# Kernel optimization log

Measured on AMD Instinct MI355X. Metric: run time of the kernel, lower is better.

## Reference

```python
import jax, jax.numpy as jnp
import numpy as np

NUM_HEADS = 8
WINDOW = 3
LOCAL_LEN = WINDOW * WINDOW
SR_RATIO = 8


def _normalize(v, eps=1e-12):
    n = jnp.linalg.norm(v, axis=-1, keepdims=True)
    return v / jnp.maximum(n, eps)


def _layernorm(v, g, b, eps=1e-5):
    m = v.mean(-1, keepdims=True)
    var = ((v - m) ** 2).mean(-1, keepdims=True)
    return (v - m) / jnp.sqrt(var + eps) * g + b


def _unfold3(x, H, W):
    # x: [B, C, H, W] -> [B, C, 9, H*W]  (kernel 3, pad 1, stride 1; torch nn.Unfold layout)
    B, C = x.shape[0], x.shape[1]
    xp = jnp.pad(x, ((0, 0), (0, 0), (1, 1), (1, 1)))
    patches = jnp.stack([xp[:, :, di:di + H, dj:dj + W]
                         for di in range(WINDOW) for dj in range(WINDOW)], axis=2)
    return patches.reshape(B, C, LOCAL_LEN, H * W)


def _forward(x, relative_coords_table, seq_length_scale, q_w, q_b, kv_w, kv_b,
             temperature, query_embedding, sr_w, sr_b, norm_g, norm_b,
             cpb_fc1_w, cpb_fc1_b, cpb_fc2_w, cpb_fc2_b,
             rel_bias_local, learnable_tokens, learnable_bias,
             proj_w, proj_b, relative_pos_index, padding_mask, H, W):
    B, N, C = x.shape
    hd = C // NUM_HEADS
    pool_H, pool_W = H // SR_RATIO, W // SR_RATIO
    pool_len = pool_H * pool_W

    # ---- queries ----
    q = (x @ q_w.T + q_b).reshape(B, N, NUM_HEADS, hd).transpose(0, 2, 1, 3)  # [B,h,N,d]
    q_norm = _normalize(q)
    q_scaled = (q_norm + query_embedding) * jax.nn.softplus(temperature) * seq_length_scale

    # ---- local k/v via unfold ----
    kv = x @ kv_w.T + kv_b  # [B,N,2C]
    k_loc = _normalize(kv[..., :C].reshape(B, N, NUM_HEADS, hd)).reshape(B, N, C)
    kv_img = jnp.concatenate([k_loc, kv[..., C:]], -1).transpose(0, 2, 1).reshape(B, 2 * C, H, W)
    kv_unf = _unfold3(kv_img, H, W).reshape(B, 2 * NUM_HEADS, hd, LOCAL_LEN, N)
    kv_unf = kv_unf.transpose(0, 1, 4, 2, 3)  # [B,2h,N,d,9]
    k_local, v_local = kv_unf[:, :NUM_HEADS], kv_unf[:, NUM_HEADS:]

    attn_local = jnp.einsum('bhnd,bhndl->bhnl', q_scaled, k_local) + rel_bias_local[:, None, :]
    attn_local = jnp.where(padding_mask, -jnp.inf, attn_local)

    # ---- pooled global k/v ----
    x_img = x.transpose(0, 2, 1).reshape(B, C, H, W)
    x_sr = jax.nn.gelu(jnp.einsum('oc,bchw->bohw', sr_w, x_img) + sr_b[None, :, None, None],
                       approximate=False)
    x_pool = x_sr.reshape(B, C, pool_H, SR_RATIO, pool_W, SR_RATIO).mean((3, 5))
    x_pool = x_pool.reshape(B, C, pool_len).transpose(0, 2, 1)
    x_pool = _layernorm(x_pool, norm_g, norm_b)
    kv_p = (x_pool @ kv_w.T + kv_b).reshape(B, pool_len, 2 * NUM_HEADS, hd).transpose(0, 2, 1, 3)
    k_pool, v_pool = kv_p[:, :NUM_HEADS], kv_p[:, NUM_HEADS:]

    # ---- continuous relative position bias (extrapolation path) ----
    cpb = jax.nn.relu(relative_coords_table @ cpb_fc1_w.T + cpb_fc1_b) @ cpb_fc2_w.T + cpb_fc2_b  # [T,h]
    pool_bias = cpb[relative_pos_index].reshape(N, pool_len, NUM_HEADS).transpose(2, 0, 1)  # [h,N,P]

    attn_pool = jnp.einsum('bhnd,bhpd->bhnp', q_scaled, _normalize(k_pool)) + pool_bias

    attn = jax.nn.softmax(jnp.concatenate([attn_local, attn_pool], -1), axis=-1)
    a_loc, a_pool = attn[..., :LOCAL_LEN], attn[..., LOCAL_LEN:]

    lt = jnp.einsum('bhnd,hdl->bhnl', q_norm, learnable_tokens) + learnable_bias + a_loc
    x_local = jnp.einsum('bhnl,bhndl->bhnd', lt, v_local)
    x_p = jnp.einsum('bhnp,bhpd->bhnd', a_pool, v_pool)
    out = (x_local + x_p).transpose(0, 2, 1, 3).reshape(B, N, C)
    return out @ proj_w.T + proj_b


def setup_inputs() -> dict:
    key = jax.random.key(0)
    B, H, W, C = 4, 64, 64, 256
    N = H * W
    hd = C // NUM_HEADS
    pool_H, pool_W = H // SR_RATIO, W // SR_RATIO
    pool_len = pool_H * pool_W

    # padding mask + per-query valid window length (get_seqlen_and_mask)
    ii, jj = np.meshgrid(np.arange(H), np.arange(W), indexing='ij')
    cols = []
    for di in range(WINDOW):
        for dj in range(WINDOW):
            ni, nj = ii + di - 1, jj + dj - 1
            cols.append(((ni < 0) | (ni >= H) | (nj < 0) | (nj >= W)).reshape(-1))
    padding_mask = np.stack(cols, -1)  # [N, 9], True = outside image
    local_len = (~padding_mask).sum(-1, keepdims=True).astype(np.float32)
    seq_length_scale = np.log(local_len + pool_len)  # [N, 1]

    # get_relative_position_cpb((H,W), (pool_H,pool_W))
    axis_q = np.arange(H, dtype=np.float64)
    axis_k = axis_q.reshape(pool_H, SR_RATIO).mean(-1)
    kh, kw = np.meshgrid(axis_k, axis_k, indexing='ij')
    qh, qw = np.meshgrid(axis_q, axis_q, indexing='ij')
    rel_h = (qh.ravel()[:, None] - kh.ravel()[None, :]) / (H - 1) * 8
    rel_w = (qw.ravel()[:, None] - kw.ravel()[None, :]) / (W - 1) * 8
    rel = np.stack([rel_h, rel_w], -1).reshape(-1, 2)
    table, idx = np.unique(rel, axis=0, return_inverse=True)
    table = np.sign(table) * np.log2(np.abs(table) + 1.0) / np.log2(8.0)

    ks = jax.random.split(key, 12)

    def nrm(k, shape, std=0.02):
        return jax.random.normal(k, shape, jnp.float32) * std

    return {
        'x': jax.random.normal(ks[0], (B, N, C), jnp.float32),
        'relative_coords_table': jnp.asarray(table, jnp.float32),
        'seq_length_scale': jnp.asarray(seq_length_scale, jnp.float32),
        'q_w': nrm(ks[1], (C, C)), 'q_b': jnp.zeros((C,), jnp.float32),
        'kv_w': nrm(ks[2], (2 * C, C)), 'kv_b': jnp.zeros((2 * C,), jnp.float32),
        'temperature': jnp.full((NUM_HEADS, 1, 1), float(np.log(np.expm1(1.0 / 0.24))), jnp.float32),
        'query_embedding': nrm(ks[3], (NUM_HEADS, 1, hd)),
        'sr_w': nrm(ks[4], (C, C)), 'sr_b': jnp.zeros((C,), jnp.float32),
        'norm_g': jnp.ones((C,), jnp.float32), 'norm_b': jnp.zeros((C,), jnp.float32),
        'cpb_fc1_w': nrm(ks[5], (512, 2), 0.1), 'cpb_fc1_b': jnp.zeros((512,), jnp.float32),
        'cpb_fc2_w': nrm(ks[6], (NUM_HEADS, 512)), 'cpb_fc2_b': jnp.zeros((NUM_HEADS,), jnp.float32),
        'rel_bias_local': nrm(ks[7], (NUM_HEADS, LOCAL_LEN), 0.0004),
        'learnable_tokens': nrm(ks[8], (NUM_HEADS, hd, LOCAL_LEN)),
        'learnable_bias': jnp.zeros((NUM_HEADS, 1, LOCAL_LEN), jnp.float32),
        'proj_w': nrm(ks[9], (C, C)), 'proj_b': jnp.zeros((C,), jnp.float32),
        'relative_pos_index': jnp.asarray(idx, jnp.int32),
        'padding_mask': jnp.asarray(padding_mask),
        'H': H, 'W': W,
    }


def reference(x, relative_coords_table, seq_length_scale, q_w, q_b, kv_w, kv_b,
              temperature, query_embedding, sr_w, sr_b, norm_g, norm_b,
              cpb_fc1_w, cpb_fc1_b, cpb_fc2_w, cpb_fc2_b,
              rel_bias_local, learnable_tokens, learnable_bias,
              proj_w, proj_b, relative_pos_index, padding_mask, H, W):
    return _forward(x, relative_coords_table, seq_length_scale, q_w, q_b, kv_w, kv_b,
                    temperature, query_embedding, sr_w, sr_b, norm_g, norm_b,
                    cpb_fc1_w, cpb_fc1_b, cpb_fc2_w, cpb_fc2_b,
                    rel_bias_local, learnable_tokens, learnable_bias,
                    proj_w, proj_b, relative_pos_index, padding_mask, H, W)
```

## Files before the change

### kernel.cpp

```cpp
#include <hip/hip_runtime.h>
#include <math.h>


typedef unsigned short ushort_t;
typedef __attribute__((ext_vector_type(8))) _Float16 half8;
typedef __attribute__((ext_vector_type(2))) _Float16 half2_t;
typedef __attribute__((ext_vector_type(4))) float f32x4;

static __device__ __forceinline__ ushort_t f2h(float f) {
    _Float16 h = (_Float16)f;
    return *(ushort_t*)&h;
}

static __device__ __forceinline__ float fdot2f(half2_t a, half2_t b, float c) {
#if __has_builtin(__builtin_amdgcn_fdot2)
    return __builtin_amdgcn_fdot2(a, b, c, false);
#else
    return (float)a[0] * (float)b[0] + (float)a[1] * (float)b[1] + c;
#endif
}

#define GLOAD16(g, l)                                                        \
    __builtin_amdgcn_global_load_lds(                                        \
        (const __attribute__((address_space(1))) unsigned int*)(g),          \
        (__attribute__((address_space(3))) unsigned int*)(l), 16, 0, 0)

template <int TM>
__global__ __launch_bounds__(256) void mfma_hgemm(
    const ushort_t* __restrict__ Ag, const ushort_t* __restrict__ Bg,
    const float* __restrict__ bias, float* __restrict__ out0,
    ushort_t* __restrict__ qh_out, ushort_t* __restrict__ kvh,
    ushort_t* __restrict__ xsrh, int mode)
{
    const int K = 256;
    const int IM = TM / 32;
    __shared__ ushort_t Ah[TM * 32];
    __shared__ ushort_t Bh[64 * 32];

    const int t = threadIdx.x;
    const int w = t >> 6;
    const int lane = t & 63;
    const int bm = blockIdx.y * TM;
    const int bn = blockIdx.x * 64;
    const int wm = (w >> 1) * (TM / 2);
    const int wn = (w & 1) * 32;

    f32x4 acc[IM][2];
#pragma unroll
    for (int i = 0; i < IM; ++i)
#pragma unroll
        for (int j = 0; j < 2; ++j) acc[i][j] = f32x4{0.f, 0.f, 0.f, 0.f};

    const int lrow = t >> 2;
    const int lk8  = (t & 3) * 8;

    for (int k0 = 0; k0 < K; k0 += 32) {
#pragma unroll
        for (int r = 0; r < TM / 64; ++r) {
            GLOAD16(Ag + (size_t)(bm + r * 64 + lrow) * K + k0 + lk8,
                    &Ah[(unsigned)(r * 64 + (w * 16)) * 32]);
        }
        GLOAD16(Bg + (size_t)(bn + lrow) * K + k0 + lk8,
                &Bh[(unsigned)(w * 16) * 32]);
        __syncthreads();

        const int fr = lane & 15;
        const int fq = (lane >> 4) * 8;
        half8 af[IM], bf[2];
#pragma unroll
        for (int i = 0; i < IM; ++i)
            af[i] = *(const half8*)&Ah[(wm + i * 16 + fr) * 32 + fq];
#pragma unroll
        for (int j = 0; j < 2; ++j)
            bf[j] = *(const half8*)&Bh[(wn + j * 16 + fr) * 32 + fq];
#pragma unroll
        for (int i = 0; i < IM; ++i)
#pragma unroll
            for (int j = 0; j < 2; ++j)
                acc[i][j] = __builtin_amdgcn_mfma_f32_16x16x32_f16(af[i], bf[j], acc[i][j], 0, 0, 0);
        __syncthreads();
    }

    const int fr = lane & 15;
    const int q4 = (lane >> 4) * 4;
#pragma unroll
    for (int i = 0; i < IM; ++i) {
#pragma unroll
        for (int r = 0; r < 4; ++r) {
            const int row = bm + wm + i * 16 + q4 + r;
            const int col0 = bn + wn + fr;
            const int col1 = col0 + 16;
            float v0 = acc[i][0][r] + bias[col0];
            float v1 = acc[i][1][r] + bias[col1];
            if (mode == 0) {
                if (col0 < 256) {
                    qh_out[(size_t)row * 256 + col0] = f2h(v0);
                    qh_out[(size_t)row * 256 + col1] = f2h(v1);
                } else if (col0 < 512) {
                    float ss = v0 * v0 + v1 * v1;
                    ss += __shfl_xor(ss, 1); ss += __shfl_xor(ss, 2);
                    ss += __shfl_xor(ss, 4); ss += __shfl_xor(ss, 8);
                    const float invn = 1.0f / fmaxf(sqrtf(ss), 1e-12f);
                    kvh[(size_t)row * 512 + (col0 - 256)] = f2h(v0 * invn);
                    kvh[(size_t)row * 512 + (col1 - 256)] = f2h(v1 * invn);
                } else if (col0 < 768) {
                    kvh[(size_t)row * 512 + (col0 - 256)] = f2h(v0);
                    kvh[(size_t)row * 512 + (col1 - 256)] = f2h(v1);
                } else {
                    v0 = 0.5f * v0 * (1.0f + erff(v0 * 0.70710678118654752f));
                    v1 = 0.5f * v1 * (1.0f + erff(v1 * 0.70710678118654752f));
                    xsrh[(size_t)row * 256 + (col0 - 768)] = f2h(v0);
                    xsrh[(size_t)row * 256 + (col1 - 768)] = f2h(v1);
                }
            } else {
                out0[(size_t)row * 256 + col0] = v0;
                out0[(size_t)row * 256 + col1] = v1;
            }
        }
    }
}

__global__ __launch_bounds__(256) void prep(
    const float4* __restrict__ x, ushort4* __restrict__ xh, int n4,
    const float* __restrict__ qw, const float* __restrict__ kvw,
    const float* __restrict__ srw, const float* __restrict__ pw,
    const float* __restrict__ qb, const float* __restrict__ kvb,
    const float* __restrict__ srb,
    ushort_t* __restrict__ Wall, ushort_t* __restrict__ Pw,
    float* __restrict__ ball)
{
    int idx = blockIdx.x * 256 + threadIdx.x;
    if (idx < n4) {
        float4 v = x[idx];
        ushort4 h;
        h.x = f2h(v.x); h.y = f2h(v.y); h.z = f2h(v.z); h.w = f2h(v.w);
        xh[idx] = h;
    }
    if (idx < 262144) {
        int nn = idx >> 8, k = idx & 255;
        float a;
        if (nn < 256)      a = qw[nn * 256 + k];
        else if (nn < 768) a = kvw[(nn - 256) * 256 + k];
        else               a = srw[(nn - 768) * 256 + k];
        Wall[idx] = f2h(a);
    }
    if (idx < 65536) Pw[idx] = f2h(pw[idx]);
    if (idx < 1024) {
        float bv;
        if (idx < 256)      bv = qb[idx];
        else if (idx < 768) bv = kvb[idx - 256];
        else                bv = srb[idx - 768];
        ball[idx] = bv;
    }
}

__global__ __launch_bounds__(256) void bias_expand_t(
    const int* __restrict__ rpi, const float* __restrict__ cpbT,
    float* __restrict__ pbias)
{
    int idx = blockIdx.x * 256 + threadIdx.x;
    int h = idx >> 18;
    int np = idx & 262143;
    pbias[idx] = cpbT[(size_t)rpi[np] * 8 + h];
}

#define BM 64
#define BN 64
#define BKK 16
__global__ __launch_bounds__(256) void gemm_bias_act(
    const float* __restrict__ A, const float* __restrict__ Wt,
    const float* __restrict__ bias, float* __restrict__ Cmat,
    int M, int N, int K, int act)
{
    __shared__ float As[BKK][BM + 4];
    __shared__ float Bs[BKK][BN + 4];
    const int tid = threadIdx.x;
    const int bm = blockIdx.y * BM;
    const int bn = blockIdx.x * BN;
    const int tr = (tid >> 4) << 2;
    const int tc = (tid & 15) << 2;
    const int lr = tid >> 2;
    const int lc = (tid & 3) << 2;
    float acc[4][4] = {{0.f}};

    for (int k0 = 0; k0 < K; k0 += BKK) {
        float4 av = *(const float4*)(A  + (size_t)(bm + lr) * K + k0 + lc);
        float4 wv = *(const float4*)(Wt + (size_t)(bn + lr) * K + k0 + lc);
        As[lc + 0][lr] = av.x; As[lc + 1][lr] = av.y;
        As[lc + 2][lr] = av.z; As[lc + 3][lr] = av.w;
        Bs[lc + 0][lr] = wv.x; Bs[lc + 1][lr] = wv.y;
        Bs[lc + 2][lr] = wv.z; Bs[lc + 3][lr] = wv.w;
        __syncthreads();
#pragma unroll
        for (int kk = 0; kk < BKK; ++kk) {
            float4 a  = *(const float4*)&As[kk][tr];
            float4 bq = *(const float4*)&Bs[kk][tc];
            float av4[4] = {a.x, a.y, a.z, a.w};
            float bv4[4] = {bq.x, bq.y, bq.z, bq.w};
#pragma unroll
            for (int ii = 0; ii < 4; ++ii)
#pragma unroll
                for (int jj = 0; jj < 4; ++jj)
                    acc[ii][jj] = fmaf(av4[ii], bv4[jj], acc[ii][jj]);
        }
        __syncthreads();
    }
#pragma unroll
    for (int ii = 0; ii < 4; ++ii) {
        int m = bm + tr + ii;
#pragma unroll
        for (int jj = 0; jj < 4; ++jj) {
            int nn = bn + tc + jj;
            float v = acc[ii][jj] + bias[nn];
            if (act == 1) v = 0.5f * v * (1.0f + erff(v * 0.70710678118654752f));
            Cmat[(size_t)m * N + nn] = v;
        }
    }
}

__global__ __launch_bounds__(256) void headnorm(float* __restrict__ buf, int rowStride)
{
    size_t row = blockIdx.x;
    int tid = threadIdx.x;
    float* p = buf + row * (size_t)rowStride + tid;
    float v = *p;
    float ss = v * v;
#pragma unroll
    for (int off = 16; off; off >>= 1) ss += __shfl_xor(ss, off, 32);
    *p = v / fmaxf(sqrtf(ss), 1e-12f);
}

__global__ __launch_bounds__(256) void pool_ln(
    const ushort_t* __restrict__ xsr, const float* __restrict__ g,
    const float* __restrict__ be, float* __restrict__ xpool, int Hh, int Ww)
{
    const int C = 256;
    const int Nn = Hh * Ww;
    int b = blockIdx.x >> 6;
    int pidx = blockIdx.x & 63;
    int ph = pidx >> 3, pw = pidx & 7;
    int tid = threadIdx.x;
    float s = 0.f;
    for (int si = 0; si < 8; ++si) {
        int i = ph * 8 + si;
        const ushort_t* rowp = xsr + ((size_t)b * Nn + (size_t)i * Ww + pw * 8) * C + tid;
#pragma unroll
        for (int sj = 0; sj < 8; ++sj)
            s += (float)(*(const _Float16*)&rowp[(size_t)sj * C]);
    }
    s *= (1.f / 64.f);
    __shared__ float red[256];
    red[tid] = s; __syncthreads();
    for (int st = 128; st; st >>= 1) { if (tid < st) red[tid] += red[tid + st]; __syncthreads(); }
    float mean = red[0] * (1.f / 256.f);
    __syncthreads();
    float dv = s - mean;
    red[tid] = dv * dv; __syncthreads();
    for (int st = 128; st; st >>= 1) { if (tid < st) red[tid] += red[tid + st]; __syncthreads(); }
    float var = red[0] * (1.f / 256.f);
    xpool[(size_t)blockIdx.x * C + tid] = dv * rsqrtf(var + 1e-5f) * g[tid] + be[tid];
}

__global__ __launch_bounds__(256) void cpb_mlp_v2(
    const float* __restrict__ table, const float* __restrict__ w1,
    const float* __restrict__ b1, const float* __restrict__ w2,
    const float* __restrict__ b2, float* __restrict__ outc, int T)
{
    const int wv = threadIdx.x >> 6;
    const int lane = threadIdx.x & 63;
    const int row = blockIdx.x * 4 + wv;
    if (row >= T) return;
    const float t0 = table[(size_t)row * 2];
    const float t1 = table[(size_t)row * 2 + 1];
    const int base = lane * 8;

    const float4* w1p = (const float4*)(w1 + (size_t)base * 2);
    float4 wa = w1p[0], wb = w1p[1], wc = w1p[2], wd = w1p[3];
    float4 ba = *(const float4*)(b1 + base);
    float4 bb = *(const float4*)(b1 + base + 4);
    float h[8];
    h[0] = fmaxf(fmaf(t1, wa.y, fmaf(t0, wa.x, ba.x)), 0.f);
    h[1] = fmaxf(fmaf(t1, wa.w, fmaf(t0, wa.z, ba.y)), 0.f);
    h[2] = fmaxf(fmaf(t1, wb.y, fmaf(t0, wb.x, ba.z)), 0.f);
    h[3] = fmaxf(fmaf(t1, wb.w, fmaf(t0, wb.z, ba.w)), 0.f);
    h[4] = fmaxf(fmaf(t1, wc.y, fmaf(t0, wc.x, bb.x)), 0.f);
    h[5] = fmaxf(fmaf(t1, wc.w, fmaf(t0, wc.z, bb.y)), 0.f);
    h[6] = fmaxf(fmaf(t1, wd.y, fmaf(t0, wd.x, bb.z)), 0.f);
    h[7] = fmaxf(fmaf(t1, wd.w, fmaf(t0, wd.z, bb.w)), 0.f);

#pragma unroll
    for (int hh = 0; hh < 8; ++hh) {
        const float4* w2p = (const float4*)(w2 + (size_t)hh * 512 + base);
        float4 p0 = w2p[0], p1 = w2p[1];
        float s = h[0]*p0.x + h[1]*p0.y + h[2]*p0.z + h[3]*p0.w
                + h[4]*p1.x + h[5]*p1.y + h[6]*p1.z + h[7]*p1.w;
#pragma unroll
        for (int off = 1; off <= 32; off <<= 1) s += __shfl_xor(s, off);
        if (lane == 0) outc[(size_t)row * 8 + hh] = s + b2[hh];
    }
}

__global__ __launch_bounds__(256) void attn_v7(
    const ushort_t* __restrict__ qh_g,
    const ushort_t* __restrict__ kvh,
    const float* __restrict__ kvp,
    const float* __restrict__ pbias,
    const float* __restrict__ sls, const float* __restrict__ temp,
    const float* __restrict__ qe, const float* __restrict__ rbl,
    const float* __restrict__ ltok, const float* __restrict__ lbias,
    ushort_t* __restrict__ attno_hf)
{
    const int h = blockIdx.y, b = blockIdx.z;
    const int t = threadIdx.x;

    __shared__ half8 kp_s[64][4];
    __shared__ half8 vp_s[64][4];
    __shared__ float lts[9][32];
    __shared__ float rbl_s[9], lb_s[9], qe_s[32];

    {
        const int p = t >> 2;
        const int g4 = t & 3;
        const float* g = kvp + ((size_t)(b * 64 + p)) * 512 + h * 32 + g4 * 8;
        float4 ka = *(const float4*)(g + 0);
        float4 kb = *(const float4*)(g + 4);
        float4 va = *(const float4*)(g + 256);
        float4 vb = *(const float4*)(g + 260);
        half8 kh, vh;
        kh[0]=(_Float16)ka.x; kh[1]=(_Float16)ka.y; kh[2]=(_Float16)ka.z; kh[3]=(_Float16)ka.w;
        kh[4]=(_Float16)kb.x; kh[5]=(_Float16)kb.y; kh[6]=(_Float16)kb.z; kh[7]=(_Float16)kb.w;
        vh[0]=(_Float16)va.x; vh[1]=(_Float16)va.y; vh[2]=(_Float16)va.z; vh[3]=(_Float16)va.w;
        vh[4]=(_Float16)vb.x; vh[5]=(_Float16)vb.y; vh[6]=(_Float16)vb.z; vh[7]=(_Float16)vb.w;
        kp_s[p][g4] = kh;
        vp_s[p][g4] = vh;
        for (int u = t; u < 288; u += 256) lts[u % 9][u / 9] = ltok[h * 288 + u];
        if (t < 9)  { rbl_s[t] = rbl[h * 9 + t]; lb_s[t] = lbias[h * 9 + t]; }
        if (t >= 64 && t < 96) qe_s[t - 64] = qe[h * 32 + (t - 64)];
    }
    __syncthreads();

    const int w = t >> 6;
    const int lane = t & 63;
    const int qi = lane >> 2;
    const int g4 = lane & 3;
    const int co = g4 * 8;
    const int i = blockIdx.x;
    const int j = w * 16 + qi;
    const int n = i * 64 + j;
    const size_t gq = (size_t)b * 4096 + n;

    const float tm = temp[h];
    const float sp = (tm > 20.f) ? tm : log1pf(expf(tm));

    float qv[8];
    {
        const half8 q8 = *(const half8*)(qh_g + gq * 256 + h * 32 + co);
        float ss = 0.f;
#pragma unroll
        for (int d = 0; d < 8; ++d) { qv[d] = (float)q8[d]; ss += qv[d] * qv[d]; }
        ss += __shfl_xor(ss, 1);
        ss += __shfl_xor(ss, 2);
        const float invn = 1.0f / fmaxf(sqrtf(ss), 1e-12f);
#pragma unroll
        for (int d = 0; d < 8; ++d) qv[d] *= invn;
    }

    float lt[9];
#pragma unroll
    for (int l = 0; l < 9; ++l) {
        float dl = 0.f;
        const float4* lw = (const float4*)&lts[l][co];
#pragma unroll
        for (int c4 = 0; c4 < 2; ++c4) {
            float4 w4 = lw[c4];
            dl += qv[4*c4+0]*w4.x + qv[4*c4+1]*w4.y + qv[4*c4+2]*w4.z + qv[4*c4+3]*w4.w;
        }
        dl += __shfl_xor(dl, 1);
        dl += __shfl_xor(dl, 2);
        lt[l] = dl + lb_s[l];
    }

    const float scal = sp * sls[n];
    half2_t qh[4];
#pragma unroll
    for (int c = 0; c < 4; ++c) {
        float a = (qv[2*c+0] + qe_s[co + 2*c+0]) * scal;
        float bq = (qv[2*c+1] + qe_s[co + 2*c+1]) * scal;
        qh[c] = half2_t{(_Float16)a, (_Float16)bq};
    }

    float sl[9];
#pragma unroll
    for (int l = 0; l < 9; ++l) {
        const int di = l / 3 - 1, dj = l % 3 - 1;
        const int ii = i + di;
        const int jn = j + dj;
        const bool ok = (ii >= 0) && (ii < 64) && (jn >= 0) && (jn < 64);
        const int ic = max(min(ii, 63), 0);
        const int jc = max(min(jn, 63), 0);
        const half8 k8 = *(const half8*)(kvh + ((size_t)(b * 4096 + ic * 64 + jc)) * 512 + h * 32 + co);
        float dk = 0.f;
        dk = fdot2f(qh[0], __builtin_shufflevector(k8, k8, 0, 1), dk);
        dk = fdot2f(qh[1], __builtin_shufflevector(k8, k8, 2, 3), dk);
        dk = fdot2f(qh[2], __builtin_shufflevector(k8, k8, 4, 5), dk);
        dk = fdot2f(qh[3], __builtin_shufflevector(k8, k8, 6, 7), dk);
        dk += __shfl_xor(dk, 1);
        dk += __shfl_xor(dk, 2);
        sl[l] = ok ? (dk + rbl_s[l]) : -INFINITY;
    }

    float m = sl[0];
#pragma unroll
    for (int l = 1; l < 9; ++l) m = fmaxf(m, sl[l]);

    half2_t oh[4];
#pragma unroll
    for (int c = 0; c < 4; ++c) oh[c] = half2_t{(_Float16)0.f, (_Float16)0.f};
    float Z = 0.f;
    const float* plane = pbias + ((size_t)h << 18) + (size_t)n * 64;

    for (int cch = 0; cch < 8; ++cch) {
        float s8[8];
        float4 pb0 = *(const float4*)(plane + cch * 8);
        float4 pb1 = *(const float4*)(plane + cch * 8 + 4);
        const float pbv[8] = {pb0.x, pb0.y, pb0.z, pb0.w, pb1.x, pb1.y, pb1.z, pb1.w};
#pragma unroll
        for (int k = 0; k < 8; ++k) {
            const int p = cch * 8 + k;
            const half8 k8 = kp_s[p][g4];
            float acc = 0.f;
            acc = fdot2f(qh[0], __builtin_shufflevector(k8, k8, 0, 1), acc);
            acc = fdot2f(qh[1], __builtin_shufflevector(k8, k8, 2, 3), acc);
            acc = fdot2f(qh[2], __builtin_shufflevector(k8, k8, 4, 5), acc);
            acc = fdot2f(qh[3], __builtin_shufflevector(k8, k8, 6, 7), acc);
            acc += __shfl_xor(acc, 1);
            acc += __shfl_xor(acc, 2);
            s8[k] = acc + pbv[k];
        }
        float cmax = s8[0];
#pragma unroll
        for (int k = 1; k < 8; ++k) cmax = fmaxf(cmax, s8[k]);
        const float m_new = fmaxf(m, cmax);
        const float factor = __expf(m - m_new);
        Z *= factor;
        const _Float16 fh = (_Float16)factor;
        const half2_t f2 = half2_t{fh, fh};
#pragma unroll
        for (int c = 0; c < 4; ++c) oh[c] *= f2;
        m = m_new;
#pragma unroll
        for (int k = 0; k < 8; ++k) {
            const float a = __expf(s8[k] - m);
            Z += a;
            const _Float16 ah = (_Float16)a;
            const half2_t a2 = half2_t{ah, ah};
            const half8 v8 = vp_s[cch * 8 + k][g4];
            oh[0] = a2 * __builtin_shufflevector(v8, v8, 0, 1) + oh[0];
            oh[1] = a2 * __builtin_shufflevector(v8, v8, 2, 3) + oh[1];
            oh[2] = a2 * __builtin_shufflevector(v8, v8, 4, 5) + oh[2];
            oh[3] = a2 * __builtin_shufflevector(v8, v8, 6, 7) + oh[3];
        }
    }

#pragma unroll
    for (int l = 0; l < 9; ++l) { sl[l] = __expf(sl[l] - m); Z += sl[l]; }

#pragma unroll
    for (int l = 0; l < 9; ++l) {
        const int di = l / 3 - 1, dj = l % 3 - 1;
        const int ii = i + di;
        const int jn = j + dj;
        const bool ok = (ii >= 0) && (ii < 64) && (jn >= 0) && (jn < 64);
        const int ic = max(min(ii, 63), 0);
        const int jc = max(min(jn, 63), 0);
        const float coef = ok ? (sl[l] + lt[l] * Z) : 0.f;
        const half8 v8 = *(const half8*)(kvh + ((size_t)(b * 4096 + ic * 64 + jc)) * 512 + 256 + h * 32 + co);
        const _Float16 ch = (_Float16)coef;
        const half2_t c2 = half2_t{ch, ch};
        oh[0] = c2 * __builtin_shufflevector(v8, v8, 0, 1) + oh[0];
        oh[1] = c2 * __builtin_shufflevector(v8, v8, 2, 3) + oh[1];
        oh[2] = c2 * __builtin_shufflevector(v8, v8, 4, 5) + oh[2];
        oh[3] = c2 * __builtin_shufflevector(v8, v8, 6, 7) + oh[3];
    }

    const float invZ = 1.0f / Z;
    ushort4* outp = (ushort4*)(attno_hf + gq * 256 + h * 32 + co);
#pragma unroll
    for (int c4 = 0; c4 < 2; ++c4) {
        ushort4 u;
        u.x = f2h((float)oh[2*c4+0][0] * invZ);
        u.y = f2h((float)oh[2*c4+0][1] * invZ);
        u.z = f2h((float)oh[2*c4+1][0] * invZ);
        u.w = f2h((float)oh[2*c4+1][1] * invZ);
        outp[c4] = u;
    }
}

extern "C" void kernel_launch(void* const* d_in, const int* in_sizes, int n_in,
                              void* d_out, int out_size, void* d_ws, size_t ws_size,
                              hipStream_t stream)
{
    const float* x    = (const float*)d_in[0];
    const float* tbl  = (const float*)d_in[1];
    const float* sls  = (const float*)d_in[2];
    const float* q_w  = (const float*)d_in[3];
    const float* q_b  = (const float*)d_in[4];
    const float* kv_w = (const float*)d_in[5];
    const float* kv_b = (const float*)d_in[6];
    const float* temp = (const float*)d_in[7];
    const float* qe   = (const float*)d_in[8];
    const float* sr_w = (const float*)d_in[9];
    const float* sr_b = (const float*)d_in[10];
    const float* ng   = (const float*)d_in[11];
    const float* nb   = (const float*)d_in[12];
    const float* f1w  = (const float*)d_in[13];
    const float* f1b  = (const float*)d_in[14];
    const float* f2w  = (const float*)d_in[15];
    const float* f2b  = (const float*)d_in[16];
    const float* rbl  = (const float*)d_in[17];
    const float* ltok = (const float*)d_in[18];
    const float* lbias= (const float*)d_in[19];
    const float* pw   = (const float*)d_in[20];
    const float* pb   = (const float*)d_in[21];
    const int*   rpi  = (const int*)d_in[22];

    const int C = 256, Hh = 64, Ww = 64, Nn = Hh * Ww;
    const int B = in_sizes[0] / (Nn * C);
    const int T = in_sizes[1] / 2;
    const int M = B * Nn;

    float* ws = (float*)d_ws;
    size_t o = 0;
    ushort_t* qh   = (ushort_t*)(ws + o); o += (size_t)M * C / 2;
    ushort_t* kvh  = (ushort_t*)(ws + o); o += (size_t)M * C;
    ushort_t* xsrh = (ushort_t*)(ws + o); o += (size_t)M * C / 2;
    float* xpool = ws + o; o += (size_t)B * 64 * C;
    float* kvp   = ws + o; o += (size_t)B * 64 * 2 * C;
    float* cpbB  = ws + o; o += (size_t)T * 8;
    float* pbias = ws + o; o += (size_t)8 * Nn * 64;
    ushort_t* xh   = (ushort_t*)(ws + o); o += (size_t)M * C / 2;
    ushort_t* Wall = (ushort_t*)(ws + o); o += 1024 * 256 / 2;
    ushort_t* Pwh  = (ushort_t*)(ws + o); o += 256 * 256 / 2;
    float* ball = ws + o; o += 1024;
    ushort_t* attno_hf = xh;

    dim3 blk(256);
    const int n4x = M * C / 4;

    prep<<<(n4x + 255) / 256, blk, 0, stream>>>(
        (const float4*)x, (ushort4*)xh, n4x,
        q_w, kv_w, sr_w, pw, q_b, kv_b, sr_b, Wall, Pwh, ball);
    mfma_hgemm<128><<<dim3(16, M / 128), blk, 0, stream>>>(
        xh, Wall, ball, nullptr, qh, kvh, xsrh, 0);
    pool_ln<<<B * 64, blk, 0, stream>>>(xsrh, ng, nb, xpool, Hh, Ww);
    gemm_bias_act<<<dim3(2 * C / BN, (B * 64) / BM), blk, 0, stream>>>(xpool, kv_w, kv_b, kvp, B * 64, 2 * C, C, 0);
    headnorm<<<B * 64, blk, 0, stream>>>(kvp, 2 * C);
    cpb_mlp_v2<<<(T + 3) / 4, blk, 0, stream>>>(tbl, f1w, f1b, f2w, f2b, cpbB, T);
    bias_expand_t<<<(8 * Nn * 64) / 256, blk, 0, stream>>>(rpi, cpbB, pbias);
    attn_v7<<<dim3(64, 8, B), blk, 0, stream>>>(
        qh, kvh, kvp, pbias, sls, temp, qe, rbl, ltok, lbias, attno_hf);
    mfma_hgemm<64><<<dim3(4, M / 64), blk, 0, stream>>>(
        attno_hf, Pwh, pb, (float*)d_out, nullptr, nullptr, nullptr, 1);
}
```

Before: 232.8 us.

## Fuse CPB MLP into prep, gather position bias in attention, MFMA pooled KV

Merges the CPB MLP into the prep kernel as extra blocks. It removes the bias_expand kernel and its large fp32 bias plane by gathering relative-position bias into shared memory inside the attention kernel. The pooled KV projection and head normalisation move onto the fp16 MFMA GEMM with a new epilogue mode, and pool_ln now writes fp16. Shuffle reductions are replaced by DPP adds. These changes cut kernel launches and global traffic, at the cost of an indexed gather per attention block and lower precision for the pooled KV.

```diff
diff --git a/kernel.cpp b/kernel.cpp
--- a/kernel.cpp
+++ b/kernel.cpp
@@ -18,6 +18,19 @@
 #else
     return (float)a[0] * (float)b[0] + (float)a[1] * (float)b[1] + c;
 #endif
+}
+
+template <int CTRL>
+static __device__ __forceinline__ float dpp_addf(float x) {
+    int v = __builtin_amdgcn_update_dpp(
+        0, __builtin_bit_cast(int, x), CTRL, 0xF, 0xF, true);
+    return x + __builtin_bit_cast(float, v);
+}
+static __device__ __forceinline__ float quad_sumf(float x) {
+    return dpp_addf<0x4E>(dpp_addf<0xB1>(x));
+}
+static __device__ __forceinline__ float sum16f(float x) {
+    return dpp_addf<0x128>(dpp_addf<0x124>(quad_sumf(x)));
 }
 
 #define GLOAD16(g, l)                                                        \
@@ -97,9 +110,7 @@
                     qh_out[(size_t)row * 256 + col0] = f2h(v0);
                     qh_out[(size_t)row * 256 + col1] = f2h(v1);
                 } else if (col0 < 512) {
-                    float ss = v0 * v0 + v1 * v1;
-                    ss += __shfl_xor(ss, 1); ss += __shfl_xor(ss, 2);
-                    ss += __shfl_xor(ss, 4); ss += __shfl_xor(ss, 8);
+                    const float ss = sum16f(v0 * v0 + v1 * v1);
                     const float invn = 1.0f / fmaxf(sqrtf(ss), 1e-12f);
                     kvh[(size_t)row * 512 + (col0 - 256)] = f2h(v0 * invn);
                     kvh[(size_t)row * 512 + (col1 - 256)] = f2h(v1 * invn);
@@ -112,6 +123,14 @@
                     xsrh[(size_t)row * 256 + (col0 - 768)] = f2h(v0);
                     xsrh[(size_t)row * 256 + (col1 - 768)] = f2h(v1);
                 }
+            } else if (mode == 2) {
+                if (col0 < 256) {
+                    const float ss = sum16f(v0 * v0 + v1 * v1);
+                    const float invn = 1.0f / fmaxf(sqrtf(ss), 1e-12f);
+                    v0 *= invn; v1 *= invn;
+                }
+                kvh[(size_t)row * 512 + col0] = f2h(v0);
+                kvh[(size_t)row * 512 + col1] = f2h(v1);
             } else {
                 out0[(size_t)row * 256 + col0] = v0;
                 out0[(size_t)row * 256 + col1] = v1;
@@ -120,15 +139,54 @@
     }
 }
 
-__global__ __launch_bounds__(256) void prep(
-    const float4* __restrict__ x, ushort4* __restrict__ xh, int n4,
+__global__ __launch_bounds__(256) void prep_cpb(
+    const float4* __restrict__ x, ushort4* __restrict__ xh, int n4, int nprep,
     const float* __restrict__ qw, const float* __restrict__ kvw,
     const float* __restrict__ srw, const float* __restrict__ pw,
     const float* __restrict__ qb, const float* __restrict__ kvb,
     const float* __restrict__ srb,
     ushort_t* __restrict__ Wall, ushort_t* __restrict__ Pw,
-    float* __restrict__ ball)
+    float* __restrict__ ball,
+    const float* __restrict__ table, const float* __restrict__ w1,
+    const float* __restrict__ b1, const float* __restrict__ w2,
+    const float* __restrict__ b2, float* __restrict__ outc, int T)
 {
+    if (blockIdx.x >= nprep) {
+        const int wv = threadIdx.x >> 6;
+        const int lane = threadIdx.x & 63;
+        const int row = (blockIdx.x - nprep) * 4 + wv;
+        if (row >= T) return;
+        const float t0 = table[(size_t)row * 2];
+        const float t1 = table[(size_t)row * 2 + 1];
+        const int base = lane * 8;
+
+        const float4* w1p = (const float4*)(w1 + (size_t)base * 2);
+        float4 wa = w1p[0], wb = w1p[1], wc = w1p[2], wd = w1p[3];
+        float4 ba = *(const float4*)(b1 + base);
+        float4 bb = *(const float4*)(b1 + base + 4);
+        float h[8];
+        h[0] = fmaxf(fmaf(t1, wa.y, fmaf(t0, wa.x, ba.x)), 0.f);
+        h[1] = fmaxf(fmaf(t1, wa.w, fmaf(t0, wa.z, ba.y)), 0.f);
+        h[2] = fmaxf(fmaf(t1, wb.y, fmaf(t0, wb.x, ba.z)), 0.f);
+        h[3] = fmaxf(fmaf(t1, wb.w, fmaf(t0, wb.z, ba.w)), 0.f);
+        h[4] = fmaxf(fmaf(t1, wc.y, fmaf(t0, wc.x, bb.x)), 0.f);
+        h[5] = fmaxf(fmaf(t1, wc.w, fmaf(t0, wc.z, bb.y)), 0.f);
+        h[6] = fmaxf(fmaf(t1, wd.y, fmaf(t0, wd.x, bb.z)), 0.f);
+        h[7] = fmaxf(fmaf(t1, wd.w, fmaf(t0, wd.z, bb.w)), 0.f);
+
+#pragma unroll
+        for (int hh = 0; hh < 8; ++hh) {
+            const float4* w2p = (const float4*)(w2 + (size_t)hh * 512 + base);
+            float4 p0 = w2p[0], p1 = w2p[1];
+            float s = h[0]*p0.x + h[1]*p0.y + h[2]*p0.z + h[3]*p0.w
+                    + h[4]*p1.x + h[5]*p1.y + h[6]*p1.z + h[7]*p1.w;
+#pragma unroll
+            for (int off = 1; off <= 32; off <<= 1) s += __shfl_xor(s, off);
+            if (lane == 0) outc[(size_t)row * 8 + hh] = s + b2[hh];
+        }
+        return;
+    }
+
     int idx = blockIdx.x * 256 + threadIdx.x;
     if (idx < n4) {
         float4 v = x[idx];
@@ -154,85 +212,9 @@
     }
 }
 
-__global__ __launch_bounds__(256) void bias_expand_t(
-    const int* __restrict__ rpi, const float* __restrict__ cpbT,
-    float* __restrict__ pbias)
-{
-    int idx = blockIdx.x * 256 + threadIdx.x;
-    int h = idx >> 18;
-    int np = idx & 262143;
-    pbias[idx] = cpbT[(size_t)rpi[np] * 8 + h];
-}
-
-#define BM 64
-#define BN 64
-#define BKK 16
-__global__ __launch_bounds__(256) void gemm_bias_act(
-    const float* __restrict__ A, const float* __restrict__ Wt,
-    const float* __restrict__ bias, float* __restrict__ Cmat,
-    int M, int N, int K, int act)
-{
-    __shared__ float As[BKK][BM + 4];
-    __shared__ float Bs[BKK][BN + 4];
-    const int tid = threadIdx.x;
-    const int bm = blockIdx.y * BM;
-    const int bn = blockIdx.x * BN;
-    const int tr = (tid >> 4) << 2;
-    const int tc = (tid & 15) << 2;
-    const int lr = tid >> 2;
-    const int lc = (tid & 3) << 2;
-    float acc[4][4] = {{0.f}};
-
-    for (int k0 = 0; k0 < K; k0 += BKK) {
-        float4 av = *(const float4*)(A  + (size_t)(bm + lr) * K + k0 + lc);
-        float4 wv = *(const float4*)(Wt + (size_t)(bn + lr) * K + k0 + lc);
-        As[lc + 0][lr] = av.x; As[lc + 1][lr] = av.y;
-        As[lc + 2][lr] = av.z; As[lc + 3][lr] = av.w;
-        Bs[lc + 0][lr] = wv.x; Bs[lc + 1][lr] = wv.y;
-        Bs[lc + 2][lr] = wv.z; Bs[lc + 3][lr] = wv.w;
-        __syncthreads();
-#pragma unroll
-        for (int kk = 0; kk < BKK; ++kk) {
-            float4 a  = *(const float4*)&As[kk][tr];
-            float4 bq = *(const float4*)&Bs[kk][tc];
-            float av4[4] = {a.x, a.y, a.z, a.w};
-            float bv4[4] = {bq.x, bq.y, bq.z, bq.w};
-#pragma unroll
-            for (int ii = 0; ii < 4; ++ii)
-#pragma unroll
-                for (int jj = 0; jj < 4; ++jj)
-                    acc[ii][jj] = fmaf(av4[ii], bv4[jj], acc[ii][jj]);
-        }
-        __syncthreads();
-    }
-#pragma unroll
-    for (int ii = 0; ii < 4; ++ii) {
-        int m = bm + tr + ii;
-#pragma unroll
-        for (int jj = 0; jj < 4; ++jj) {
-            int nn = bn + tc + jj;
-            float v = acc[ii][jj] + bias[nn];
-            if (act == 1) v = 0.5f * v * (1.0f + erff(v * 0.70710678118654752f));
-            Cmat[(size_t)m * N + nn] = v;
-        }
-    }
-}
-
-__global__ __launch_bounds__(256) void headnorm(float* __restrict__ buf, int rowStride)
-{
-    size_t row = blockIdx.x;
-    int tid = threadIdx.x;
-    float* p = buf + row * (size_t)rowStride + tid;
-    float v = *p;
-    float ss = v * v;
-#pragma unroll
-    for (int off = 16; off; off >>= 1) ss += __shfl_xor(ss, off, 32);
-    *p = v / fmaxf(sqrtf(ss), 1e-12f);
-}
-
 __global__ __launch_bounds__(256) void pool_ln(
     const ushort_t* __restrict__ xsr, const float* __restrict__ g,
-    const float* __restrict__ be, float* __restrict__ xpool, int Hh, int Ww)
+    const float* __restrict__ be, ushort_t* __restrict__ xpool, int Hh, int Ww)
 {
     const int C = 256;
     const int Nn = Hh * Ww;
@@ -258,53 +240,15 @@
     red[tid] = dv * dv; __syncthreads();
     for (int st = 128; st; st >>= 1) { if (tid < st) red[tid] += red[tid + st]; __syncthreads(); }
     float var = red[0] * (1.f / 256.f);
-    xpool[(size_t)blockIdx.x * C + tid] = dv * rsqrtf(var + 1e-5f) * g[tid] + be[tid];
-}
-
-__global__ __launch_bounds__(256) void cpb_mlp_v2(
-    const float* __restrict__ table, const float* __restrict__ w1,
-    const float* __restrict__ b1, const float* __restrict__ w2,
-    const float* __restrict__ b2, float* __restrict__ outc, int T)
-{
-    const int wv = threadIdx.x >> 6;
-    const int lane = threadIdx.x & 63;
-    const int row = blockIdx.x * 4 + wv;
-    if (row >= T) return;
-    const float t0 = table[(size_t)row * 2];
-    const float t1 = table[(size_t)row * 2 + 1];
-    const int base = lane * 8;
-
-    const float4* w1p = (const float4*)(w1 + (size_t)base * 2);
-    float4 wa = w1p[0], wb = w1p[1], wc = w1p[2], wd = w1p[3];
-    float4 ba = *(const float4*)(b1 + base);
-    float4 bb = *(const float4*)(b1 + base + 4);
-    float h[8];
-    h[0] = fmaxf(fmaf(t1, wa.y, fmaf(t0, wa.x, ba.x)), 0.f);
-    h[1] = fmaxf(fmaf(t1, wa.w, fmaf(t0, wa.z, ba.y)), 0.f);
-    h[2] = fmaxf(fmaf(t1, wb.y, fmaf(t0, wb.x, ba.z)), 0.f);
-    h[3] = fmaxf(fmaf(t1, wb.w, fmaf(t0, wb.z, ba.w)), 0.f);
-    h[4] = fmaxf(fmaf(t1, wc.y, fmaf(t0, wc.x, bb.x)), 0.f);
-    h[5] = fmaxf(fmaf(t1, wc.w, fmaf(t0, wc.z, bb.y)), 0.f);
-    h[6] = fmaxf(fmaf(t1, wd.y, fmaf(t0, wd.x, bb.z)), 0.f);
-    h[7] = fmaxf(fmaf(t1, wd.w, fmaf(t0, wd.z, bb.w)), 0.f);
-
-#pragma unroll
-    for (int hh = 0; hh < 8; ++hh) {
-        const float4* w2p = (const float4*)(w2 + (size_t)hh * 512 + base);
-        float4 p0 = w2p[0], p1 = w2p[1];
-        float s = h[0]*p0.x + h[1]*p0.y + h[2]*p0.z + h[3]*p0.w
-                + h[4]*p1.x + h[5]*p1.y + h[6]*p1.z + h[7]*p1.w;
-#pragma unroll
-        for (int off = 1; off <= 32; off <<= 1) s += __shfl_xor(s, off);
-        if (lane == 0) outc[(size_t)row * 8 + hh] = s + b2[hh];
-    }
-}
-
-__global__ __launch_bounds__(256) void attn_v7(
+    xpool[(size_t)blockIdx.x * C + tid] = f2h(dv * rsqrtf(var + 1e-5f) * g[tid] + be[tid]);
+}
+
+__global__ __launch_bounds__(256) void attn_v8(
     const ushort_t* __restrict__ qh_g,
     const ushort_t* __restrict__ kvh,
-    const float* __restrict__ kvp,
-    const float* __restrict__ pbias,
+    const ushort_t* __restrict__ kvph,
+    const int* __restrict__ rpi,
+    const float* __restrict__ cpbB,
     const float* __restrict__ sls, const float* __restrict__ temp,
     const float* __restrict__ qe, const float* __restrict__ rbl,
     const float* __restrict__ ltok, const float* __restrict__ lbias,
@@ -312,27 +256,25 @@
 {
     const int h = blockIdx.y, b = blockIdx.z;
     const int t = threadIdx.x;
+    const int i = blockIdx.x;
 
     __shared__ half8 kp_s[64][4];
     __shared__ half8 vp_s[64][4];
+    __shared__ ushort_t pb_s[64][66];
     __shared__ float lts[9][32];
     __shared__ float rbl_s[9], lb_s[9], qe_s[32];
 
     {
         const int p = t >> 2;
-        const int g4 = t & 3;
-        const float* g = kvp + ((size_t)(b * 64 + p)) * 512 + h * 32 + g4 * 8;
-        float4 ka = *(const float4*)(g + 0);
-        float4 kb = *(const float4*)(g + 4);
-        float4 va = *(const float4*)(g + 256);
-        float4 vb = *(const float4*)(g + 260);
-        half8 kh, vh;
-        kh[0]=(_Float16)ka.x; kh[1]=(_Float16)ka.y; kh[2]=(_Float16)ka.z; kh[3]=(_Float16)ka.w;
-        kh[4]=(_Float16)kb.x; kh[5]=(_Float16)kb.y; kh[6]=(_Float16)kb.z; kh[7]=(_Float16)kb.w;
-        vh[0]=(_Float16)va.x; vh[1]=(_Float16)va.y; vh[2]=(_Float16)va.z; vh[3]=(_Float16)va.w;
-        vh[4]=(_Float16)vb.x; vh[5]=(_Float16)vb.y; vh[6]=(_Float16)vb.z; vh[7]=(_Float16)vb.w;
-        kp_s[p][g4] = kh;
-        vp_s[p][g4] = vh;
+        const int g4s = t & 3;
+        const ushort_t* gk = kvph + ((size_t)(b * 64 + p)) * 512 + h * 32 + g4s * 8;
+        kp_s[p][g4s] = *(const half8*)gk;
+        vp_s[p][g4s] = *(const half8*)(gk + 256);
+        const int rbase = i * 4096;
+        for (int u = t; u < 4096; u += 256) {
+            const int idx = rpi[rbase + u];
+            pb_s[u >> 6][u & 63] = f2h(cpbB[(size_t)idx * 8 + h]);
+        }
         for (int u = t; u < 288; u += 256) lts[u % 9][u / 9] = ltok[h * 288 + u];
         if (t < 9)  { rbl_s[t] = rbl[h * 9 + t]; lb_s[t] = lbias[h * 9 + t]; }
         if (t >= 64 && t < 96) qe_s[t - 64] = qe[h * 32 + (t - 64)];
@@ -344,7 +286,6 @@
     const int qi = lane >> 2;
     const int g4 = lane & 3;
     const int co = g4 * 8;
-    const int i = blockIdx.x;
     const int j = w * 16 + qi;
     const int n = i * 64 + j;
     const size_t gq = (size_t)b * 4096 + n;
@@ -358,8 +299,7 @@
         float ss = 0.f;
 #pragma unroll
         for (int d = 0; d < 8; ++d) { qv[d] = (float)q8[d]; ss += qv[d] * qv[d]; }
-        ss += __shfl_xor(ss, 1);
-        ss += __shfl_xor(ss, 2);
+        ss = quad_sumf(ss);
         const float invn = 1.0f / fmaxf(sqrtf(ss), 1e-12f);
 #pragma unroll
         for (int d = 0; d < 8; ++d) qv[d] *= invn;
@@ -375,8 +315,7 @@
             float4 w4 = lw[c4];
             dl += qv[4*c4+0]*w4.x + qv[4*c4+1]*w4.y + qv[4*c4+2]*w4.z + qv[4*c4+3]*w4.w;
         }
-        dl += __shfl_xor(dl, 1);
-        dl += __shfl_xor(dl, 2);
+        dl = quad_sumf(dl);
         lt[l] = dl + lb_s[l];
     }
 
@@ -404,8 +343,7 @@
         dk = fdot2f(qh[1], __builtin_shufflevector(k8, k8, 2, 3), dk);
         dk = fdot2f(qh[2], __builtin_shufflevector(k8, k8, 4, 5), dk);
         dk = fdot2f(qh[3], __builtin_shufflevector(k8, k8, 6, 7), dk);
-        dk += __shfl_xor(dk, 1);
-        dk += __shfl_xor(dk, 2);
+        dk = quad_sumf(dk);
         sl[l] = ok ? (dk + rbl_s[l]) : -INFINITY;
     }
 
@@ -417,13 +355,16 @@
 #pragma unroll
     for (int c = 0; c < 4; ++c) oh[c] = half2_t{(_Float16)0.f, (_Float16)0.f};
     float Z = 0.f;
-    const float* plane = pbias + ((size_t)h << 18) + (size_t)n * 64;
 
     for (int cch = 0; cch < 8; ++cch) {
         float s8[8];
-        float4 pb0 = *(const float4*)(plane + cch * 8);
-        float4 pb1 = *(const float4*)(plane + cch * 8 + 4);
-        const float pbv[8] = {pb0.x, pb0.y, pb0.z, pb0.w, pb1.x, pb1.y, pb1.z, pb1.w};
+        float pbv[8];
+#pragma unroll
+        for (int c = 0; c < 4; ++c) {
+            const half2_t p2 = *(const half2_t*)&pb_s[j][cch * 8 + 2 * c];
+            pbv[2*c]   = (float)p2[0];
+            pbv[2*c+1] = (float)p2[1];
+        }
 #pragma unroll
         for (int k = 0; k < 8; ++k) {
             const int p = cch * 8 + k;
@@ -433,8 +374,7 @@
             acc = fdot2f(qh[1], __builtin_shufflevector(k8, k8, 2, 3), acc);
             acc = fdot2f(qh[2], __builtin_shufflevector(k8, k8, 4, 5), acc);
             acc = fdot2f(qh[3], __builtin_shufflevector(k8, k8, 6, 7), acc);
-            acc += __shfl_xor(acc, 1);
-            acc += __shfl_xor(acc, 2);
+            acc = quad_sumf(acc);
             s8[k] = acc + pbv[k];
         }
         float cmax = s8[0];
@@ -531,13 +471,12 @@
 
     float* ws = (float*)d_ws;
     size_t o = 0;
-    ushort_t* qh   = (ushort_t*)(ws + o); o += (size_t)M * C / 2;
-    ushort_t* kvh  = (ushort_t*)(ws + o); o += (size_t)M * C;
-    ushort_t* xsrh = (ushort_t*)(ws + o); o += (size_t)M * C / 2;
-    float* xpool = ws + o; o += (size_t)B * 64 * C;
-    float* kvp   = ws + o; o += (size_t)B * 64 * 2 * C;
+    ushort_t* qh    = (ushort_t*)(ws + o); o += (size_t)M * C / 2;
+    ushort_t* kvh   = (ushort_t*)(ws + o); o += (size_t)M * C;
+    ushort_t* xsrh  = (ushort_t*)(ws + o); o += (size_t)M * C / 2;
+    ushort_t* xpoolh= (ushort_t*)(ws + o); o += (size_t)B * 64 * C / 2;
+    ushort_t* kvph  = (ushort_t*)(ws + o); o += (size_t)B * 64 * C;
     float* cpbB  = ws + o; o += (size_t)T * 8;
-    float* pbias = ws + o; o += (size_t)8 * Nn * 64;
     ushort_t* xh   = (ushort_t*)(ws + o); o += (size_t)M * C / 2;
     ushort_t* Wall = (ushort_t*)(ws + o); o += 1024 * 256 / 2;
     ushort_t* Pwh  = (ushort_t*)(ws + o); o += 256 * 256 / 2;
@@ -546,19 +485,20 @@
 
     dim3 blk(256);
     const int n4x = M * C / 4;
-
-    prep<<<(n4x + 255) / 256, blk, 0, stream>>>(
-        (const float4*)x, (ushort4*)xh, n4x,
-        q_w, kv_w, sr_w, pw, q_b, kv_b, sr_b, Wall, Pwh, ball);
+    const int nprep = (n4x + 255) / 256;
+    const int ncpb  = (T + 3) / 4;
+
+    prep_cpb<<<nprep + ncpb, blk, 0, stream>>>(
+        (const float4*)x, (ushort4*)xh, n4x, nprep,
+        q_w, kv_w, sr_w, pw, q_b, kv_b, sr_b, Wall, Pwh, ball,
+        tbl, f1w, f1b, f2w, f2b, cpbB, T);
     mfma_hgemm<128><<<dim3(16, M / 128), blk, 0, stream>>>(
         xh, Wall, ball, nullptr, qh, kvh, xsrh, 0);
-    pool_ln<<<B * 64, blk, 0, stream>>>(xsrh, ng, nb, xpool, Hh, Ww);
-    gemm_bias_act<<<dim3(2 * C / BN, (B * 64) / BM), blk, 0, stream>>>(xpool, kv_w, kv_b, kvp, B * 64, 2 * C, C, 0);
-    headnorm<<<B * 64, blk, 0, stream>>>(kvp, 2 * C);
-    cpb_mlp_v2<<<(T + 3) / 4, blk, 0, stream>>>(tbl, f1w, f1b, f2w, f2b, cpbB, T);
-    bias_expand_t<<<(8 * Nn * 64) / 256, blk, 0, stream>>>(rpi, cpbB, pbias);
-    attn_v7<<<dim3(64, 8, B), blk, 0, stream>>>(
-        qh, kvh, kvp, pbias, sls, temp, qe, rbl, ltok, lbias, attno_hf);
+    pool_ln<<<B * 64, blk, 0, stream>>>(xsrh, ng, nb, xpoolh, Hh, Ww);
+    mfma_hgemm<64><<<dim3(8, (B * 64) / 64), blk, 0, stream>>>(
+        xpoolh, Wall + 256 * 256, ball + 256, nullptr, nullptr, kvph, nullptr, 2);
+    attn_v8<<<dim3(64, 8, B), blk, 0, stream>>>(
+        qh, kvh, kvph, rpi, cpbB, sls, temp, qe, rbl, ltok, lbias, attno_hf);
     mfma_hgemm<64><<<dim3(4, M / 64), blk, 0, stream>>>(
         attno_hf, Pwh, pb, (float*)d_out, nullptr, nullptr, nullptr, 1);
 }
```

Measured after the change: 214.5 us. -7.9%, faster.
